# Kernel tuning notes

Hardware: AMD Instinct MI355X
Metric: run time of the kernel (lower is better)

The kernel has to match this reference:

```python
import jax, jax.numpy as jnp
import numpy as np

N_NODES = 100000
N_EDGES = 1600000
IN_F = 16
OUT_F = 64
PERIODS = 12
N_PHASE = 4


def setup_inputs() -> dict:
    key = jax.random.key(0)
    ks = jax.random.split(key, 12)
    inp = {
        'x': jax.random.normal(ks[0], (N_NODES, IN_F, PERIODS), jnp.float32),
        'edge_index': jax.random.randint(ks[1], (2, N_EDGES), 0, N_NODES, jnp.int64),
        'attn': jax.random.normal(ks[2], (PERIODS,), jnp.float32),
        'conv_z_w': jax.random.normal(ks[3], (IN_F, OUT_F), jnp.float32) * 0.1,
        'conv_z_b': jnp.zeros((OUT_F,), jnp.float32),
        'conv_r_w': jax.random.normal(ks[4], (IN_F, OUT_F), jnp.float32) * 0.1,
        'conv_r_b': jnp.zeros((OUT_F,), jnp.float32),
        'conv_h_w': jax.random.normal(ks[5], (IN_F, OUT_F), jnp.float32) * 0.1,
        'conv_h_b': jnp.zeros((OUT_F,), jnp.float32),
        'lin_z_w': jax.random.normal(ks[6], (2 * OUT_F, OUT_F), jnp.float32) * 0.1,
        'lin_z_b': jnp.zeros((OUT_F,), jnp.float32),
        'lin_r_w': jax.random.normal(ks[7], (2 * OUT_F, OUT_F), jnp.float32) * 0.1,
        'lin_r_b': jnp.zeros((OUT_F,), jnp.float32),
        'lin_h_w': jax.random.normal(ks[8], (2 * OUT_F, OUT_F), jnp.float32) * 0.1,
        'lin_h_b': jnp.zeros((OUT_F,), jnp.float32),
        'out_w': jax.random.normal(ks[9], (OUT_F, N_PHASE), jnp.float32) * 0.1,
        'out_b': jnp.zeros((N_PHASE,), jnp.float32),
    }
    return inp


def _gcn_norm(edge_index, num_nodes, dtype):
    # add self loops (fill value 1), symmetric normalization as in PyG gcn_norm
    loops = jnp.arange(num_nodes, dtype=edge_index.dtype)
    src = jnp.concatenate([edge_index[0], loops])
    dst = jnp.concatenate([edge_index[1], loops])
    deg = jax.ops.segment_sum(jnp.ones_like(dst, dtype=dtype), dst, num_segments=num_nodes)
    dinv = jnp.where(deg > 0, jax.lax.rsqrt(deg), jnp.zeros_like(deg))
    norm = dinv[src] * dinv[dst]  # [E + N]
    return src, dst, norm


def reference(x, edge_index, attn, conv_z_w, conv_z_b, conv_r_w, conv_r_b,
              conv_h_w, conv_h_b, lin_z_w, lin_z_b, lin_r_w, lin_r_b,
              lin_h_w, lin_h_b, out_w, out_b):
    N = x.shape[0]
    periods = x.shape[2]
    F_out = conv_z_w.shape[1]
    src, dst, norm = _gcn_norm(edge_index, N, x.dtype)

    def conv(Xp, W, b):
        XW = Xp @ W                                   # [N, F_out]
        msg = norm[:, None] * XW[src]                 # gather over edges
        return jax.ops.segment_sum(msg, dst, num_segments=N) + b

    probs = jax.nn.softmax(attn)
    H0 = jnp.zeros((N, F_out), x.dtype)  # A3TGCN never carries H between periods
    H_accum = jnp.zeros((N, F_out), x.dtype)
    for p in range(periods):
        Xp = x[:, :, p]
        Z = jax.nn.sigmoid(jnp.concatenate([conv(Xp, conv_z_w, conv_z_b), H0], axis=1) @ lin_z_w + lin_z_b)
        R = jax.nn.sigmoid(jnp.concatenate([conv(Xp, conv_r_w, conv_r_b), H0], axis=1) @ lin_r_w + lin_r_b)
        Ht = jnp.tanh(jnp.concatenate([conv(Xp, conv_h_w, conv_h_b), H0 * R], axis=1) @ lin_h_w + lin_h_b)
        H = Z * H0 + (1.0 - Z) * Ht
        H_accum = H_accum + probs[p] * H

    h = jax.nn.relu(H_accum)
    logits = h @ out_w + out_b
    return jax.nn.softmax(logits, axis=1)
```

## Files before the change

kernel.cpp:

```cpp
#include <hip/hip_runtime.h>
#include <math.h>

#define NN 100000
#define NE 1600000
#define PERIODS 12
#define SLOTS 48
#define NBUCK 98
#define FRAG 256
#define CAPB 128

typedef unsigned short ushort_t;
typedef __attribute__((ext_vector_type(8))) short short8;
typedef __attribute__((ext_vector_type(16))) float floatx16;

union F4S8 { float4 f; short8 s; int4 i; };

__device__ __forceinline__ ushort_t f2bf(float f) {
  unsigned u = __float_as_uint(f);
  unsigned r = u + 0x7fffu + ((u >> 16) & 1u);
  return (ushort_t)(r >> 16);
}

__device__ __forceinline__ float bflo(unsigned u) { return __uint_as_float(u << 16); }
__device__ __forceinline__ float bfhi(unsigned u) { return __uint_as_float(u & 0xffff0000u); }

__device__ __forceinline__ unsigned aoff2(unsigned e) {
  unsigned f = (e * 43691u) >> 19;
  unsigned p = e - f * 12u;
  return p * 32u + f * 2u;
}

__global__ __launch_bounds__(256) void k_part(
    const int* __restrict__ src, const int* __restrict__ dst,
    int* __restrict__ cnt_blk, int* __restrict__ part,
    const float* __restrict__ attn,
    const float* __restrict__ czw, const float* __restrict__ czb,
    const float* __restrict__ chw, const float* __restrict__ chb,
    const float* __restrict__ lzw, const float* __restrict__ lzb,
    const float* __restrict__ lhw, const float* __restrict__ lhb,
    ushort_t* __restrict__ Bz32, ushort_t* __restrict__ Bh32,
    float2* __restrict__ cb2, float* __restrict__ probs_ext) {
  if (blockIdx.x == FRAG) {
    for (int t5 = threadIdx.x; t5 < 1024; t5 += 256) {
      int f = t5 >> 6, c = t5 & 63;
      float az = 0.f, ah = 0.f;
#pragma unroll 8
      for (int k = 0; k < 64; ++k) {
        az += czw[f * 64 + k] * lzw[k * 64 + c];
        ah += chw[f * 64 + k] * lhw[k * 64 + c];
      }
      int idx = (((c >> 5) * 64) + ((f >> 3) * 32) + (c & 31)) * 8 + (f & 7);
      Bz32[idx] = f2bf(az);
      Bh32[idx] = f2bf(ah);
    }
    if (threadIdx.x < 64) {
      int t = threadIdx.x;
      float vz = lzb[t], vh = lhb[t];
      for (int k = 0; k < 64; ++k) {
        vz += czb[k] * lzw[k * 64 + t];
        vh += chb[k] * lhw[k * 64 + t];
      }
      cb2[t] = make_float2(vz, vh);
    }
    if (threadIdx.x == 0) {
      float m = -1e30f;
      for (int p = 0; p < PERIODS; ++p) m = fmaxf(m, attn[p]);
      float e[PERIODS], s = 0.f;
      for (int p = 0; p < PERIODS; ++p) { e[p] = __expf(attn[p] - m); s += e[p]; }
      float inv = 1.f / s;
      for (int r = 0; r < 32; ++r)
        probs_ext[r] = (r < 12) ? e[r] * inv : ((r < 24) ? e[r - 12] * inv : 0.f);
    }
    return;
  }
  __shared__ int cnt[NBUCK];
  int tid = threadIdx.x, blk = blockIdx.x;
  for (int c = tid; c < NBUCK; c += 256) cnt[c] = 0;
  __syncthreads();
  for (unsigned i = blk * 256u + tid; i < NE / 4; i += FRAG * 256u) {
    int4 dv = ((const int4*)dst)[i];
    int4 sv = ((const int4*)src)[i];
    int d[4] = {dv.x, dv.y, dv.z, dv.w};
    int s[4] = {sv.x, sv.y, sv.z, sv.w};
#pragma unroll
    for (int k = 0; k < 4; ++k) {
      int cls = d[k] >> 10;
      int slot = atomicAdd(&cnt[cls], 1);
      if (slot < CAPB)
        part[(size_t)(cls * FRAG + blk) * CAPB + slot] = (d[k] & 1023) | (s[k] << 10);
    }
  }
  __syncthreads();
  for (int c = tid; c < NBUCK; c += 256) cnt_blk[blk * NBUCK + c] = cnt[c];
}

__global__ __launch_bounds__(1024) void k_csr(const int* __restrict__ cnt_blk,
                                              const int* __restrict__ part,
                                              int* __restrict__ deg,
                                              int* __restrict__ csr) {
  __shared__ int fcnt[FRAG];
  __shared__ int cnt[1024];
  int b = blockIdx.x, tid = threadIdx.x;
  for (int f = tid; f < FRAG; f += 1024) {
    int c = cnt_blk[f * NBUCK + b];
    fcnt[f] = c < CAPB ? c : CAPB;
  }
  cnt[tid] = 0;
  __syncthreads();
  int g = tid >> 8, it = tid & 255;
  for (int f = g; f < FRAG; f += 4) {
    int c = fcnt[f];
    if (it < c) {
      int r = part[(size_t)(b * FRAG + f) * CAPB + it];
      int dl = r & 1023;
      int slot = atomicAdd(&cnt[dl], 1);
      if (slot < SLOTS) csr[((size_t)(b * 1024 + dl)) * SLOTS + slot] = r >> 10;
    }
  }
  __syncthreads();
  int node = b * 1024 + tid;
  if (node < NN) deg[node] = cnt[tid];
}

__global__ __launch_bounds__(256) void k_prescale(const float* __restrict__ x,
                                                  const int* __restrict__ deg,
                                                  ushort_t* __restrict__ xs) {
  int wid = threadIdx.x >> 6, l = threadIdx.x & 63;
  int n = blockIdx.x * 4 + wid;
  float dn = rsqrtf((float)(deg[n] + 1));
  const char* xb = (const char*)x;
  unsigned nb = (unsigned)n * 768u;
  float2 p = *(const float2*)(xb + nb + (unsigned)l * 8u);
  float qv = *(const float*)(xb + nb + 512u + (unsigned)l * 4u);
  char* ob = (char*)xs;
  unsigned ro = (unsigned)n * 384u;
  unsigned pk = (unsigned)f2bf(dn * p.x) | ((unsigned)f2bf(dn * p.y) << 16);
  *(unsigned*)(ob + ro + (unsigned)l * 4u) = pk;
  *(ushort_t*)(ob + ro + 256u + (unsigned)l * 2u) = f2bf(dn * qv);
}

__global__ __launch_bounds__(256) void k_main(
    const ushort_t* __restrict__ xs, const int* __restrict__ csr,
    const int* __restrict__ deg,
    const ushort_t* __restrict__ Bz32, const ushort_t* __restrict__ Bh32,
    const float2* __restrict__ cb2, const float* __restrict__ probs_ext,
    const float* __restrict__ out_w, const float* __restrict__ out_b,
    float* __restrict__ out) {
  __shared__ ushort_t Alds[4][32][16];
  int wid = __builtin_amdgcn_readfirstlane(threadIdx.x >> 6);
  int l = threadIdx.x & 63;
  int nA = blockIdx.x * 8 + wid * 2;
  int nB = nA + 1;
  char* albase = (char*)&Alds[wid][0][0];
  if (l < 16) *(int4*)(albase + 768 + l * 16) = make_int4(0, 0, 0, 0);

  const char* xb = (const char*)xs;
  unsigned offA = (unsigned)l * 4u;
  unsigned offB = 256u + (unsigned)l * 2u;

  unsigned ba = (unsigned)nA * 384u, bb = (unsigned)nB * 384u;
  unsigned sua = *(const unsigned*)(xb + ba + offA);
  unsigned sqa = *(const ushort_t*)(xb + ba + offB);
  unsigned sub = *(const unsigned*)(xb + bb + offA);
  unsigned sqb = *(const ushort_t*)(xb + bb + offB);
  float aA0 = bflo(sua), aA1 = bfhi(sua), aA2 = bflo(sqa);
  float aB0 = bflo(sub), aB1 = bfhi(sub), aB2 = bflo(sqb);

  int dA = deg[nA], dB = deg[nB];
  int cA = dA < SLOTS ? dA : SLOTS, cB = dB < SLOTS ? dB : SLOTS;
  const int* bktA = csr + (size_t)nA * SLOTS;
  const int* bktB = bktA + SLOTS;

  auto batchA = [&](int i) {
    int4 s4 = *(const int4*)(bktA + i);
    unsigned b0 = (unsigned)s4.x * 384u, b1 = (unsigned)s4.y * 384u;
    unsigned b2 = (unsigned)s4.z * 384u, b3 = (unsigned)s4.w * 384u;
    unsigned u0 = *(const unsigned*)(xb + b0 + offA), q0 = *(const ushort_t*)(xb + b0 + offB);
    unsigned u1 = *(const unsigned*)(xb + b1 + offA), q1 = *(const ushort_t*)(xb + b1 + offB);
    unsigned u2 = *(const unsigned*)(xb + b2 + offA), q2 = *(const ushort_t*)(xb + b2 + offB);
    unsigned u3 = *(const unsigned*)(xb + b3 + offA), q3 = *(const ushort_t*)(xb + b3 + offB);
    aA0 += bflo(u0); aA1 += bfhi(u0); aA2 += bflo(q0);
    aA0 += bflo(u1); aA1 += bfhi(u1); aA2 += bflo(q1);
    aA0 += bflo(u2); aA1 += bfhi(u2); aA2 += bflo(q2);
    aA0 += bflo(u3); aA1 += bfhi(u3); aA2 += bflo(q3);
  };
  auto batchB = [&](int i) {
    int4 s4 = *(const int4*)(bktB + i);
    unsigned b0 = (unsigned)s4.x * 384u, b1 = (unsigned)s4.y * 384u;
    unsigned b2 = (unsigned)s4.z * 384u, b3 = (unsigned)s4.w * 384u;
    unsigned u0 = *(const unsigned*)(xb + b0 + offA), q0 = *(const ushort_t*)(xb + b0 + offB);
    unsigned u1 = *(const unsigned*)(xb + b1 + offA), q1 = *(const ushort_t*)(xb + b1 + offB);
    unsigned u2 = *(const unsigned*)(xb + b2 + offA), q2 = *(const ushort_t*)(xb + b2 + offB);
    unsigned u3 = *(const unsigned*)(xb + b3 + offA), q3 = *(const ushort_t*)(xb + b3 + offB);
    aB0 += bflo(u0); aB1 += bfhi(u0); aB2 += bflo(q0);
    aB0 += bflo(u1); aB1 += bfhi(u1); aB2 += bflo(q1);
    aB0 += bflo(u2); aB1 += bfhi(u2); aB2 += bflo(q2);
    aB0 += bflo(u3); aB1 += bfhi(u3); aB2 += bflo(q3);
  };

  int cm = cA < cB ? cA : cB;
  int iA = 0, iB = 0;
  for (; iA + 4 <= cm; iA += 4, iB += 4) { batchA(iA); batchB(iB); }
  for (; iA + 4 <= cA; iA += 4) batchA(iA);
  for (; iB + 4 <= cB; iB += 4) batchB(iB);
  for (; iA < cA; ++iA) {
    int s = bktA[iA];
    unsigned b = (unsigned)s * 384u;
    unsigned u = *(const unsigned*)(xb + b + offA), q = *(const ushort_t*)(xb + b + offB);
    aA0 += bflo(u); aA1 += bfhi(u); aA2 += bflo(q);
  }
  for (; iB < cB; ++iB) {
    int s = bktB[iB];
    unsigned b = (unsigned)s * 384u;
    unsigned u = *(const unsigned*)(xb + b + offA), q = *(const ushort_t*)(xb + b + offB);
    aB0 += bflo(u); aB1 += bfhi(u); aB2 += bflo(q);
  }
  float dnA = rsqrtf((float)(dA + 1)), dnB = rsqrtf((float)(dB + 1));
  float yA0 = dnA * aA0, yA1 = dnA * aA1, yA2 = dnA * aA2;
  float yB0 = dnB * aB0, yB1 = dnB * aB1, yB2 = dnB * aB2;

  unsigned o0 = aoff2(2u * l), o1 = aoff2(2u * l + 1u), o2 = aoff2(128u + (unsigned)l);
  asm volatile("s_waitcnt lgkmcnt(0)" ::: "memory");
  *(ushort_t*)(albase + o0) = f2bf(yA0);
  *(ushort_t*)(albase + o1) = f2bf(yA1);
  *(ushort_t*)(albase + o2) = f2bf(yA2);
  *(ushort_t*)(albase + 384u + o0) = f2bf(yB0);
  *(ushort_t*)(albase + 384u + o1) = f2bf(yB1);
  *(ushort_t*)(albase + 384u + o2) = f2bf(yB2);
  asm volatile("s_waitcnt lgkmcnt(0)" ::: "memory");
  F4S8 afr;
  afr.f = *(const float4*)(albase + (unsigned)(l & 31) * 32u + (unsigned)(l >> 5) * 16u);

  F4S8 bz0, bz1, bh0, bh1;
  bz0.f = ((const float4*)Bz32)[l];
  bz1.f = ((const float4*)Bz32)[64 + l];
  bh0.f = ((const float4*)Bh32)[l];
  bh1.f = ((const float4*)Bh32)[64 + l];

  floatx16 zero16;
#pragma unroll
  for (int r = 0; r < 16; ++r) zero16[r] = 0.f;
  floatx16 az0 = __builtin_amdgcn_mfma_f32_32x32x16_bf16(afr.s, bz0.s, zero16, 0, 0, 0);
  floatx16 az1 = __builtin_amdgcn_mfma_f32_32x32x16_bf16(afr.s, bz1.s, zero16, 0, 0, 0);
  floatx16 ah0 = __builtin_amdgcn_mfma_f32_32x32x16_bf16(afr.s, bh0.s, zero16, 0, 0, 0);
  floatx16 ah1 = __builtin_amdgcn_mfma_f32_32x32x16_bf16(afr.s, bh1.s, zero16, 0, 0, 0);

  float2 cbv0 = cb2[l & 31], cbv1 = cb2[(l & 31) + 32];
  float prv[12];
  unsigned sby = (l & 32u) >> 1;
#pragma unroll
  for (int r = 0; r < 12; ++r) {
    const int rb = (r & 3) + 8 * (r >> 2);
    prv[r] = *(const float*)((const char*)probs_ext + rb * 4 + sby);
  }
  bool sh = (l & 32) != 0;
  float hA[2], hB[2];
#pragma unroll
  for (int t = 0; t < 2; ++t) {
    float g0 = 0.f, g1 = 0.f, g2 = 0.f;
    float2 cbv = t ? cbv1 : cbv0;
#pragma unroll
    for (int r = 0; r < 12; ++r) {
      float zz = (t ? az1[r] : az0[r]) + cbv.x;
      float hh = (t ? ah1[r] : ah0[r]) + cbv.y;
      float ez = __expf(zz);
      float e2h = __expf(2.f * hh);
      float val = (e2h - 1.f) * __builtin_amdgcn_rcpf((1.f + ez) * (e2h + 1.f));
      float c = prv[r] * val;
      if ((r >> 2) == 0) g0 += c;
      else if ((r >> 2) == 1) g1 += c;
      else g2 += c;
    }
    float pa = g0 + (sh ? 0.f : g1);
    float pb = g2 + (sh ? g1 : 0.f);
    pa += __shfl_xor(pa, 32, 64);
    pb += __shfl_xor(pb, 32, 64);
    hA[t] = fmaxf(pa, 0.f);
    hB[t] = fmaxf(pb, 0.f);
  }

  int c0 = l & 31;
  float4 w0 = ((const float4*)out_w)[c0];
  float4 w1 = ((const float4*)out_w)[c0 + 32];
  float h0 = sh ? hB[0] : hA[0];
  float h1 = sh ? hB[1] : hA[1];
  float l0 = h0 * w0.x; l0 = fmaf(h1, w1.x, l0);
  float l1 = h0 * w0.y; l1 = fmaf(h1, w1.y, l1);
  float l2 = h0 * w0.z; l2 = fmaf(h1, w1.z, l2);
  float l3 = h0 * w0.w; l3 = fmaf(h1, w1.w, l3);
#pragma unroll
  for (int o = 1; o < 32; o <<= 1) {
    l0 += __shfl_xor(l0, o, 64);
    l1 += __shfl_xor(l1, o, 64);
    l2 += __shfl_xor(l2, o, 64);
    l3 += __shfl_xor(l3, o, 64);
  }
  l0 += out_b[0]; l1 += out_b[1]; l2 += out_b[2]; l3 += out_b[3];
  float m = fmaxf(fmaxf(l0, l1), fmaxf(l2, l3));
  float e0 = __expf(l0 - m), e1 = __expf(l1 - m), e2 = __expf(l2 - m), e3 = __expf(l3 - m);
  float inv = __builtin_amdgcn_rcpf(e0 + e1 + e2 + e3);
  if (c0 < 4) {
    float v = (c0 == 0) ? e0 * inv : (c0 == 1) ? e1 * inv : (c0 == 2) ? e2 * inv : e3 * inv;
    out[(size_t)(sh ? nB : nA) * 4 + c0] = v;
  }
}

extern "C" void kernel_launch(void* const* d_in, const int* in_sizes, int n_in,
                              void* d_out, int out_size, void* d_ws, size_t ws_size,
                              hipStream_t stream) {
  const float* x    = (const float*)d_in[0];
  const int*   ei   = (const int*)d_in[1];
  const float* attn = (const float*)d_in[2];
  const float* czw  = (const float*)d_in[3];
  const float* czb  = (const float*)d_in[4];
  const float* chw  = (const float*)d_in[7];
  const float* chb  = (const float*)d_in[8];
  const float* lzw  = (const float*)d_in[9];
  const float* lzb  = (const float*)d_in[10];
  const float* lhw  = (const float*)d_in[13];
  const float* lhb  = (const float*)d_in[14];
  const float* outw = (const float*)d_in[15];
  const float* outb = (const float*)d_in[16];
  float* out = (float*)d_out;

  char* ws = (char*)d_ws;
  size_t off = 0;
  auto alloc = [&](size_t bytes) {
    void* p = ws + off;
    off += (bytes + 255) & ~(size_t)255;
    return p;
  };
  int*      deg       = (int*)alloc((size_t)NN * 4);
  int*      csr       = (int*)alloc((size_t)NN * SLOTS * 4);
  void*     shared_region = alloc((size_t)NN * 192 * 2);
  int*      part      = (int*)shared_region;
  ushort_t* xs        = (ushort_t*)shared_region;
  int*      cnt_blk   = (int*)alloc((size_t)FRAG * NBUCK * 4);
  ushort_t* Bz32      = (ushort_t*)alloc(2 * 64 * 8 * 2);
  ushort_t* Bh32      = (ushort_t*)alloc(2 * 64 * 8 * 2);
  float2*   cb2       = (float2*)alloc(64 * 8);
  float*    probs_ext = (float*)alloc(32 * 4);

  k_part<<<FRAG + 1, 256, 0, stream>>>(ei, ei + NE, cnt_blk, part,
                                       attn, czw, czb, chw, chb,
                                       lzw, lzb, lhw, lhb,
                                       Bz32, Bh32, cb2, probs_ext);
  k_csr<<<NBUCK, 1024, 0, stream>>>(cnt_blk, part, deg, csr);
  k_prescale<<<NN / 4, 256, 0, stream>>>(x, deg, xs);
  k_main<<<NN / 8, 256, 0, stream>>>(xs, csr, deg, Bz32, Bh32, cb2, probs_ext,
                                     outw, outb, out);
}
```

Measured before the change: 312.2 us.

## Merge dual-node neighbor gather into one masked loop with zero sentinel row

The gather loop in the main kernel now walks both nodes' neighbor lists in one loop up to the larger count. Indices past each list's end point at an extra zeroed sentinel row, so the separate tail loops and scalar remainders go away. The prescale kernel gets an extra block that writes that sentinel row, and the workspace grows to hold it. k_csr changes from 256-wide to 64-wide wave groups that loop over each fragment, degrees load as an int2, and one lgkmcnt wait is removed. The cost is wasted sentinel loads whenever the two degrees differ, in return for more loads in flight and less divergent control flow.

```diff
diff --git a/kernel.cpp b/kernel.cpp
--- a/kernel.cpp
+++ b/kernel.cpp
@@ -101,17 +101,18 @@
   __shared__ int fcnt[FRAG];
   __shared__ int cnt[1024];
   int b = blockIdx.x, tid = threadIdx.x;
-  for (int f = tid; f < FRAG; f += 1024) {
-    int c = cnt_blk[f * NBUCK + b];
-    fcnt[f] = c < CAPB ? c : CAPB;
+  if (tid < FRAG) {
+    int c = cnt_blk[tid * NBUCK + b];
+    fcnt[tid] = c < CAPB ? c : CAPB;
   }
   cnt[tid] = 0;
   __syncthreads();
-  int g = tid >> 8, it = tid & 255;
-  for (int f = g; f < FRAG; f += 4) {
+  int g = tid >> 6, it = tid & 63;
+  for (int f = g; f < FRAG; f += 16) {
     int c = fcnt[f];
-    if (it < c) {
-      int r = part[(size_t)(b * FRAG + f) * CAPB + it];
+    const int* frag = part + (size_t)(b * FRAG + f) * CAPB;
+    for (int i2 = it; i2 < c; i2 += 64) {
+      int r = frag[i2];
       int dl = r & 1023;
       int slot = atomicAdd(&cnt[dl], 1);
       if (slot < SLOTS) csr[((size_t)(b * 1024 + dl)) * SLOTS + slot] = r >> 10;
@@ -127,13 +128,18 @@
                                                   ushort_t* __restrict__ xs) {
   int wid = threadIdx.x >> 6, l = threadIdx.x & 63;
   int n = blockIdx.x * 4 + wid;
+  char* ob = (char*)xs;
+  unsigned ro = (unsigned)n * 384u;
+  if (n >= NN) {
+    *(unsigned*)(ob + ro + (unsigned)l * 4u) = 0u;
+    *(ushort_t*)(ob + ro + 256u + (unsigned)l * 2u) = 0;
+    return;
+  }
   float dn = rsqrtf((float)(deg[n] + 1));
   const char* xb = (const char*)x;
   unsigned nb = (unsigned)n * 768u;
   float2 p = *(const float2*)(xb + nb + (unsigned)l * 8u);
   float qv = *(const float*)(xb + nb + 512u + (unsigned)l * 4u);
-  char* ob = (char*)xs;
-  unsigned ro = (unsigned)n * 384u;
   unsigned pk = (unsigned)f2bf(dn * p.x) | ((unsigned)f2bf(dn * p.y) << 16);
   *(unsigned*)(ob + ro + (unsigned)l * 4u) = pk;
   *(ushort_t*)(ob + ro + 256u + (unsigned)l * 2u) = f2bf(dn * qv);
@@ -163,64 +169,52 @@
   unsigned sqa = *(const ushort_t*)(xb + ba + offB);
   unsigned sub = *(const unsigned*)(xb + bb + offA);
   unsigned sqb = *(const ushort_t*)(xb + bb + offB);
-  float aA0 = bflo(sua), aA1 = bfhi(sua), aA2 = bflo(sqa);
-  float aB0 = bflo(sub), aB1 = bfhi(sub), aB2 = bflo(sqb);
-
-  int dA = deg[nA], dB = deg[nB];
-  int cA = dA < SLOTS ? dA : SLOTS, cB = dB < SLOTS ? dB : SLOTS;
+  float2 pA = make_float2(bflo(sua), bfhi(sua));
+  float2 pB = make_float2(bflo(sub), bfhi(sub));
+  float qA = bflo(sqa), qB = bflo(sqb);
+
+  int2 dd = *(const int2*)(deg + nA);
+  int dA = dd.x, dB = dd.y;
+  int cA = dA < SLOTS ? dA : SLOTS;
+  int cB = dB < SLOTS ? dB : SLOTS;
+  int cm = cA > cB ? cA : cB;
   const int* bktA = csr + (size_t)nA * SLOTS;
   const int* bktB = bktA + SLOTS;
 
-  auto batchA = [&](int i) {
-    int4 s4 = *(const int4*)(bktA + i);
-    unsigned b0 = (unsigned)s4.x * 384u, b1 = (unsigned)s4.y * 384u;
-    unsigned b2 = (unsigned)s4.z * 384u, b3 = (unsigned)s4.w * 384u;
-    unsigned u0 = *(const unsigned*)(xb + b0 + offA), q0 = *(const ushort_t*)(xb + b0 + offB);
-    unsigned u1 = *(const unsigned*)(xb + b1 + offA), q1 = *(const ushort_t*)(xb + b1 + offB);
-    unsigned u2 = *(const unsigned*)(xb + b2 + offA), q2 = *(const ushort_t*)(xb + b2 + offB);
-    unsigned u3 = *(const unsigned*)(xb + b3 + offA), q3 = *(const ushort_t*)(xb + b3 + offB);
-    aA0 += bflo(u0); aA1 += bfhi(u0); aA2 += bflo(q0);
-    aA0 += bflo(u1); aA1 += bfhi(u1); aA2 += bflo(q1);
-    aA0 += bflo(u2); aA1 += bfhi(u2); aA2 += bflo(q2);
-    aA0 += bflo(u3); aA1 += bfhi(u3); aA2 += bflo(q3);
-  };
-  auto batchB = [&](int i) {
-    int4 s4 = *(const int4*)(bktB + i);
-    unsigned b0 = (unsigned)s4.x * 384u, b1 = (unsigned)s4.y * 384u;
-    unsigned b2 = (unsigned)s4.z * 384u, b3 = (unsigned)s4.w * 384u;
-    unsigned u0 = *(const unsigned*)(xb + b0 + offA), q0 = *(const ushort_t*)(xb + b0 + offB);
-    unsigned u1 = *(const unsigned*)(xb + b1 + offA), q1 = *(const ushort_t*)(xb + b1 + offB);
-    unsigned u2 = *(const unsigned*)(xb + b2 + offA), q2 = *(const ushort_t*)(xb + b2 + offB);
-    unsigned u3 = *(const unsigned*)(xb + b3 + offA), q3 = *(const ushort_t*)(xb + b3 + offB);
-    aB0 += bflo(u0); aB1 += bfhi(u0); aB2 += bflo(q0);
-    aB0 += bflo(u1); aB1 += bfhi(u1); aB2 += bflo(q1);
-    aB0 += bflo(u2); aB1 += bfhi(u2); aB2 += bflo(q2);
-    aB0 += bflo(u3); aB1 += bfhi(u3); aB2 += bflo(q3);
-  };
-
-  int cm = cA < cB ? cA : cB;
-  int iA = 0, iB = 0;
-  for (; iA + 4 <= cm; iA += 4, iB += 4) { batchA(iA); batchB(iB); }
-  for (; iA + 4 <= cA; iA += 4) batchA(iA);
-  for (; iB + 4 <= cB; iB += 4) batchB(iB);
-  for (; iA < cA; ++iA) {
-    int s = bktA[iA];
-    unsigned b = (unsigned)s * 384u;
-    unsigned u = *(const unsigned*)(xb + b + offA), q = *(const ushort_t*)(xb + b + offB);
-    aA0 += bflo(u); aA1 += bfhi(u); aA2 += bflo(q);
-  }
-  for (; iB < cB; ++iB) {
-    int s = bktB[iB];
-    unsigned b = (unsigned)s * 384u;
-    unsigned u = *(const unsigned*)(xb + b + offA), q = *(const ushort_t*)(xb + b + offB);
-    aB0 += bflo(u); aB1 += bfhi(u); aB2 += bflo(q);
-  }
+  for (int i = 0; i < cm; i += 4) {
+    int4 sa = *(const int4*)(bktA + i);
+    int4 sb = *(const int4*)(bktB + i);
+    unsigned a0 = (unsigned)((i + 0 < cA) ? sa.x : NN) * 384u;
+    unsigned a1 = (unsigned)((i + 1 < cA) ? sa.y : NN) * 384u;
+    unsigned a2 = (unsigned)((i + 2 < cA) ? sa.z : NN) * 384u;
+    unsigned a3 = (unsigned)((i + 3 < cA) ? sa.w : NN) * 384u;
+    unsigned b0 = (unsigned)((i + 0 < cB) ? sb.x : NN) * 384u;
+    unsigned b1 = (unsigned)((i + 1 < cB) ? sb.y : NN) * 384u;
+    unsigned b2 = (unsigned)((i + 2 < cB) ? sb.z : NN) * 384u;
+    unsigned b3 = (unsigned)((i + 3 < cB) ? sb.w : NN) * 384u;
+    unsigned uA0 = *(const unsigned*)(xb + a0 + offA), xA0 = *(const ushort_t*)(xb + a0 + offB);
+    unsigned uA1 = *(const unsigned*)(xb + a1 + offA), xA1 = *(const ushort_t*)(xb + a1 + offB);
+    unsigned uA2 = *(const unsigned*)(xb + a2 + offA), xA2 = *(const ushort_t*)(xb + a2 + offB);
+    unsigned uA3 = *(const unsigned*)(xb + a3 + offA), xA3 = *(const ushort_t*)(xb + a3 + offB);
+    unsigned uB0 = *(const unsigned*)(xb + b0 + offA), xB0 = *(const ushort_t*)(xb + b0 + offB);
+    unsigned uB1 = *(const unsigned*)(xb + b1 + offA), xB1 = *(const ushort_t*)(xb + b1 + offB);
+    unsigned uB2 = *(const unsigned*)(xb + b2 + offA), xB2 = *(const ushort_t*)(xb + b2 + offB);
+    unsigned uB3 = *(const unsigned*)(xb + b3 + offA), xB3 = *(const ushort_t*)(xb + b3 + offB);
+    pA += make_float2(bflo(uA0), bfhi(uA0)); qA += bflo(xA0);
+    pA += make_float2(bflo(uA1), bfhi(uA1)); qA += bflo(xA1);
+    pA += make_float2(bflo(uA2), bfhi(uA2)); qA += bflo(xA2);
+    pA += make_float2(bflo(uA3), bfhi(uA3)); qA += bflo(xA3);
+    pB += make_float2(bflo(uB0), bfhi(uB0)); qB += bflo(xB0);
+    pB += make_float2(bflo(uB1), bfhi(uB1)); qB += bflo(xB1);
+    pB += make_float2(bflo(uB2), bfhi(uB2)); qB += bflo(xB2);
+    pB += make_float2(bflo(uB3), bfhi(uB3)); qB += bflo(xB3);
+  }
+
   float dnA = rsqrtf((float)(dA + 1)), dnB = rsqrtf((float)(dB + 1));
-  float yA0 = dnA * aA0, yA1 = dnA * aA1, yA2 = dnA * aA2;
-  float yB0 = dnB * aB0, yB1 = dnB * aB1, yB2 = dnB * aB2;
+  float yA0 = dnA * pA.x, yA1 = dnA * pA.y, yA2 = dnA * qA;
+  float yB0 = dnB * pB.x, yB1 = dnB * pB.y, yB2 = dnB * qB;
 
   unsigned o0 = aoff2(2u * l), o1 = aoff2(2u * l + 1u), o2 = aoff2(128u + (unsigned)l);
-  asm volatile("s_waitcnt lgkmcnt(0)" ::: "memory");
   *(ushort_t*)(albase + o0) = f2bf(yA0);
   *(ushort_t*)(albase + o1) = f2bf(yA1);
   *(ushort_t*)(albase + o2) = f2bf(yA2);
@@ -332,7 +326,7 @@
   };
   int*      deg       = (int*)alloc((size_t)NN * 4);
   int*      csr       = (int*)alloc((size_t)NN * SLOTS * 4);
-  void*     shared_region = alloc((size_t)NN * 192 * 2);
+  void*     shared_region = alloc((size_t)(NN + 4) * 192 * 2);
   int*      part      = (int*)shared_region;
   ushort_t* xs        = (ushort_t*)shared_region;
   int*      cnt_blk   = (int*)alloc((size_t)FRAG * NBUCK * 4);
@@ -346,7 +340,7 @@
                                        lzw, lzb, lhw, lhb,
                                        Bz32, Bh32, cb2, probs_ext);
   k_csr<<<NBUCK, 1024, 0, stream>>>(cnt_blk, part, deg, csr);
-  k_prescale<<<NN / 4, 256, 0, stream>>>(x, deg, xs);
+  k_prescale<<<NN / 4 + 1, 256, 0, stream>>>(x, deg, xs);
   k_main<<<NN / 8, 256, 0, stream>>>(xs, csr, deg, Bz32, Bh32, cb2, probs_ext,
                                      outw, outb, out);
 }
```

Result: no change. 306.2 us (-1.9%).

## Fuse degree-based prescale of x into CSR build kernel

Applied to the files above, without the earlier changes.

The prescale pass that normalizes x by rsqrt(deg+1) and converts it to bf16 now runs inside the CSR kernel, reading degrees straight from shared-memory counters. This removes a separate launch and the global round trip of deg. The CSR fragment loop is regrouped to 16 wave-sized groups, and part and xs get separate buffers because they can no longer alias. The catch is that only 98 blocks now handle the whole x conversion, so parallelism for that step is much lower. It also removes one s_waitcnt in k_main and loads the two degrees as a single int2.

```diff
diff --git a/kernel.cpp b/kernel.cpp
--- a/kernel.cpp
+++ b/kernel.cpp
@@ -97,21 +97,24 @@
 __global__ __launch_bounds__(1024) void k_csr(const int* __restrict__ cnt_blk,
                                               const int* __restrict__ part,
                                               int* __restrict__ deg,
-                                              int* __restrict__ csr) {
+                                              int* __restrict__ csr,
+                                              const float* __restrict__ x,
+                                              ushort_t* __restrict__ xs) {
   __shared__ int fcnt[FRAG];
   __shared__ int cnt[1024];
   int b = blockIdx.x, tid = threadIdx.x;
-  for (int f = tid; f < FRAG; f += 1024) {
-    int c = cnt_blk[f * NBUCK + b];
-    fcnt[f] = c < CAPB ? c : CAPB;
+  if (tid < FRAG) {
+    int c = cnt_blk[tid * NBUCK + b];
+    fcnt[tid] = c < CAPB ? c : CAPB;
   }
   cnt[tid] = 0;
   __syncthreads();
-  int g = tid >> 8, it = tid & 255;
-  for (int f = g; f < FRAG; f += 4) {
+  int g = tid >> 6, it = tid & 63;
+  for (int f = g; f < FRAG; f += 16) {
     int c = fcnt[f];
-    if (it < c) {
-      int r = part[(size_t)(b * FRAG + f) * CAPB + it];
+    const int* frag = part + (size_t)(b * FRAG + f) * CAPB;
+    for (int i2 = it; i2 < c; i2 += 64) {
+      int r = frag[i2];
       int dl = r & 1023;
       int slot = atomicAdd(&cnt[dl], 1);
       if (slot < SLOTS) csr[((size_t)(b * 1024 + dl)) * SLOTS + slot] = r >> 10;
@@ -120,23 +123,28 @@
   __syncthreads();
   int node = b * 1024 + tid;
   if (node < NN) deg[node] = cnt[tid];
-}
-
-__global__ __launch_bounds__(256) void k_prescale(const float* __restrict__ x,
-                                                  const int* __restrict__ deg,
-                                                  ushort_t* __restrict__ xs) {
-  int wid = threadIdx.x >> 6, l = threadIdx.x & 63;
-  int n = blockIdx.x * 4 + wid;
-  float dn = rsqrtf((float)(deg[n] + 1));
+
+  int w = g, l = it;
+  char* ob = (char*)xs;
   const char* xb = (const char*)x;
-  unsigned nb = (unsigned)n * 768u;
-  float2 p = *(const float2*)(xb + nb + (unsigned)l * 8u);
-  float qv = *(const float*)(xb + nb + 512u + (unsigned)l * 4u);
-  char* ob = (char*)xs;
-  unsigned ro = (unsigned)n * 384u;
-  unsigned pk = (unsigned)f2bf(dn * p.x) | ((unsigned)f2bf(dn * p.y) << 16);
-  *(unsigned*)(ob + ro + (unsigned)l * 4u) = pk;
-  *(ushort_t*)(ob + ro + 256u + (unsigned)l * 2u) = f2bf(dn * qv);
+#pragma unroll 1
+  for (int j = 0; j < 64; ++j) {
+    int n = b * 1024 + w * 64 + j;
+    if (n >= NN + 4) break;
+    unsigned ro = (unsigned)n * 384u;
+    if (n >= NN) {
+      *(unsigned*)(ob + ro + (unsigned)l * 4u) = 0u;
+      *(ushort_t*)(ob + ro + 256u + (unsigned)l * 2u) = 0;
+      continue;
+    }
+    float dn = rsqrtf((float)(cnt[w * 64 + j] + 1));
+    unsigned nb = (unsigned)n * 768u;
+    float2 p = *(const float2*)(xb + nb + (unsigned)l * 8u);
+    float qv = *(const float*)(xb + nb + 512u + (unsigned)l * 4u);
+    unsigned pk = (unsigned)f2bf(dn * p.x) | ((unsigned)f2bf(dn * p.y) << 16);
+    *(unsigned*)(ob + ro + (unsigned)l * 4u) = pk;
+    *(ushort_t*)(ob + ro + 256u + (unsigned)l * 2u) = f2bf(dn * qv);
+  }
 }
 
 __global__ __launch_bounds__(256) void k_main(
@@ -166,7 +174,8 @@
   float aA0 = bflo(sua), aA1 = bfhi(sua), aA2 = bflo(sqa);
   float aB0 = bflo(sub), aB1 = bfhi(sub), aB2 = bflo(sqb);
 
-  int dA = deg[nA], dB = deg[nB];
+  int2 dd = *(const int2*)(deg + nA);
+  int dA = dd.x, dB = dd.y;
   int cA = dA < SLOTS ? dA : SLOTS, cB = dB < SLOTS ? dB : SLOTS;
   const int* bktA = csr + (size_t)nA * SLOTS;
   const int* bktB = bktA + SLOTS;
@@ -220,7 +229,6 @@
   float yB0 = dnB * aB0, yB1 = dnB * aB1, yB2 = dnB * aB2;
 
   unsigned o0 = aoff2(2u * l), o1 = aoff2(2u * l + 1u), o2 = aoff2(128u + (unsigned)l);
-  asm volatile("s_waitcnt lgkmcnt(0)" ::: "memory");
   *(ushort_t*)(albase + o0) = f2bf(yA0);
   *(ushort_t*)(albase + o1) = f2bf(yA1);
   *(ushort_t*)(albase + o2) = f2bf(yA2);
@@ -332,9 +340,8 @@
   };
   int*      deg       = (int*)alloc((size_t)NN * 4);
   int*      csr       = (int*)alloc((size_t)NN * SLOTS * 4);
-  void*     shared_region = alloc((size_t)NN * 192 * 2);
-  int*      part      = (int*)shared_region;
-  ushort_t* xs        = (ushort_t*)shared_region;
+  int*      part      = (int*)alloc((size_t)NBUCK * FRAG * CAPB * 4);
+  ushort_t* xs        = (ushort_t*)alloc((size_t)(NN + 4) * 192 * 2);
   int*      cnt_blk   = (int*)alloc((size_t)FRAG * NBUCK * 4);
   ushort_t* Bz32      = (ushort_t*)alloc(2 * 64 * 8 * 2);
   ushort_t* Bh32      = (ushort_t*)alloc(2 * 64 * 8 * 2);
@@ -345,8 +352,7 @@
                                        attn, czw, czb, chw, chb,
                                        lzw, lzb, lhw, lhb,
                                        Bz32, Bh32, cb2, probs_ext);
-  k_csr<<<NBUCK, 1024, 0, stream>>>(cnt_blk, part, deg, csr);
-  k_prescale<<<NN / 4, 256, 0, stream>>>(x, deg, xs);
+  k_csr<<<NBUCK, 1024, 0, stream>>>(cnt_blk, part, deg, csr, x, xs);
   k_main<<<NN / 8, 256, 0, stream>>>(xs, csr, deg, Bz32, Bh32, cb2, probs_ext,
                                      outw, outb, out);
 }
```

After: 348.5 us. 1.12x slower.
